# Kernel tuning notes

Measured on AMD Instinct MI355X. Metric: run time of the kernel, lower is better.

Reference implementation:

```python
import jax, jax.numpy as jnp
import numpy as np


def setup_inputs() -> dict:
    key = jax.random.key(0)
    ks = jax.random.split(key, 7)
    B, T, D, H, O = 64, 512, 256, 1024, 256
    s = 0.02  # small init scale for numerical stability of the recurrence
    return {
        "x": jax.random.normal(ks[0], (B, T, D), dtype=jnp.float32),
        "W_ih": jax.random.normal(ks[1], (4 * H, D), dtype=jnp.float32) * s,
        "W_hh": jax.random.normal(ks[2], (4 * H, H), dtype=jnp.float32) * s,
        "b_ih": jax.random.normal(ks[3], (4 * H,), dtype=jnp.float32) * s,
        "b_hh": jax.random.normal(ks[4], (4 * H,), dtype=jnp.float32) * s,
        "W_out": jax.random.normal(ks[5], (O, H), dtype=jnp.float32) * s,
        "b_out": jax.random.normal(ks[6], (O,), dtype=jnp.float32) * s,
    }


def reference(x, W_ih, W_hh, b_ih, b_hh, W_out, b_out):
    # x: [B, T, D]. Faithful to torch nn.LSTMCell gate order (i, f, g, o)
    # followed by a per-step Linear projection, future=0 path.
    B, T, D = x.shape
    H = W_hh.shape[1]

    # Precompute input contributions for all timesteps in one GEMM: [T, B, 4H]
    xg = jnp.einsum('btd,gd->tbg', x, W_ih) + b_ih + b_hh

    def step(carry, xg_t):
        h, c = carry
        gates = xg_t + h @ W_hh.T  # [B, 4H]
        i, f, g, o = jnp.split(gates, 4, axis=-1)
        i = jax.nn.sigmoid(i)
        f = jax.nn.sigmoid(f)
        g = jnp.tanh(g)
        o = jax.nn.sigmoid(o)
        c = f * c + i * g
        h = o * jnp.tanh(c)
        return (h, c), h

    h0 = jnp.zeros((B, H), dtype=x.dtype)
    c0 = jnp.zeros((B, H), dtype=x.dtype)
    _, hs = jax.lax.scan(step, (h0, c0), xg)  # hs: [T, B, H]

    # Per-step Linear, batched over time: [B, T, O]
    outputs = jnp.einsum('tbh,oh->bto', hs, W_out) + b_out
    return outputs
```

## Files before the change

kernel.cpp:

```cpp
#include <hip/hip_runtime.h>

#define B_ 64
#define T_ 512
#define D_ 256
#define H_ 1024
#define O_ 256
#define KTOT 1280
#define NBLK 256
#define NTHR 256

typedef __bf16 bf16x8 __attribute__((ext_vector_type(8)));
typedef float f32x4 __attribute__((ext_vector_type(4)));

__device__ __forceinline__ unsigned short f2bf(float f) {
    unsigned int u = __builtin_bit_cast(unsigned int, f);
    unsigned int r = (u + 0x7fffu + ((u >> 16) & 1u)) >> 16;
    return (unsigned short)r;
}
__device__ __forceinline__ float sigmoid_f(float x) { return 1.f / (1.f + __expf(-x)); }
__device__ __forceinline__ float tanh_f(float x)    { return 1.f - 2.f / (1.f + __expf(2.f * x)); }

#define ARR_OFF 0
#define RLS_OFF (T_ * NBLK)
#define SYNC_INTS (T_ * NBLK + T_ * 128)

__global__ void zero_sync(int* s) { s[blockIdx.x * 256 + threadIdx.x] = 0; }

__global__ __launch_bounds__(256) void pack_weights(
    const float* __restrict__ Wih, const float* __restrict__ Whh,
    const float* __restrict__ bih, const float* __restrict__ bhh,
    const float* __restrict__ Wout,
    unsigned short* __restrict__ Wp, float* __restrict__ bpk,
    unsigned short* __restrict__ Wo)
{
    int bid = blockIdx.x, tid = threadIdx.x;
    if (bid < 4096) {
        int g = bid & 3, j = (bid >> 2) & 3, hc = (bid >> 4) * 4 + j;
        int row = g * 1024 + hc;
        for (int e = tid; e < KTOT; e += 256) {
            float v = (e < D_) ? Wih[(size_t)row * D_ + e] : Whh[(size_t)row * H_ + (e - D_)];
            Wp[(size_t)bid * KTOT + e] = f2bf(v);
        }
        if (tid == 0) bpk[bid] = bih[row] + bhh[row];
    } else {
        int r = bid - 4096;
        for (int e = tid; e < H_; e += 256)
            Wo[(size_t)r * H_ + e] = f2bf(Wout[(size_t)r * H_ + e]);
    }
}

__global__ __launch_bounds__(256) void x_pack(const float* __restrict__ x,
                                              unsigned short* __restrict__ xt)
{
    int bid = blockIdx.x;
    int b = bid >> 9, t = bid & 511;
    int d = threadIdx.x;
    xt[((size_t)t * B_ + b) * D_ + d] = f2bf(x[(size_t)bid * D_ + d]);
}

__global__ __launch_bounds__(NTHR, 1) void lstm_scan(
    const unsigned short* __restrict__ Wp, const float* __restrict__ bpk,
    const unsigned short* __restrict__ xt, unsigned short* __restrict__ hs,
    int* __restrict__ sync)
{
    const int tid  = threadIdx.x;
    const int w    = tid >> 6, lane = tid & 63;
    const int blk  = blockIdx.x;
    const int n    = lane & 15, kg = lane >> 4;
    const int gq   = n & 3;
    const int hcol = blk * 4 + (n >> 2);
    const int m0   = w * 16;

    bf16x8 wf[40];
    {
        const bf16x8* wp8 = (const bf16x8*)(Wp + (size_t)(blk * 16 + n) * KTOT + kg * 8);
        #pragma unroll
        for (int kk = 0; kk < 40; ++kk) wf[kk] = wp8[kk * 4];
    }
    #pragma unroll
    for (int kk = 0; kk < 40; ++kk) asm volatile("" : "+v"(wf[kk]));

    const float bias = bpk[blk * 16 + n];

    float cc[4] = {0.f, 0.f, 0.f, 0.f};

    for (int t = 0; t < T_; ++t) {
        f32x4 ac[4];
        f32x4 z = {0.f, 0.f, 0.f, 0.f};
        ac[0] = z; ac[1] = z; ac[2] = z; ac[3] = z;

        {
            const bf16x8* ax = (const bf16x8*)(xt + ((size_t)t * B_ + m0 + n) * D_ + kg * 8);
            #pragma unroll
            for (int kk = 0; kk < 8; ++kk) {
                bf16x8 a = ax[kk * 4];
                ac[kk & 3] = __builtin_amdgcn_mfma_f32_16x16x32_bf16(a, wf[kk], ac[kk & 3], 0, 0, 0);
            }
        }

        if (t > 0) {
            const bool selfrel = (w == 0) && (blk == ((t - 1) & (NBLK - 1)));
            if (!selfrel) {
                const int* rw = sync + RLS_OFF + (size_t)(t - 1) * 128 + (((blk << 2) + w) & 7) * 16;
                while (__hip_atomic_load(rw, __ATOMIC_RELAXED, __HIP_MEMORY_SCOPE_AGENT) == 0) {}
            }

            const bf16x8* ah = (const bf16x8*)(hs + ((size_t)(t - 1) * B_ + m0 + n) * H_ + kg * 8);
            #pragma unroll
            for (int kk = 8; kk < 40; ++kk) {
                bf16x8 a = ah[(kk - 8) * 4];
                ac[kk & 3] = __builtin_amdgcn_mfma_f32_16x16x32_bf16(a, wf[kk], ac[kk & 3], 0, 0, 0);
            }
        }

        f32x4 g4 = (ac[0] + ac[1]) + (ac[2] + ac[3]);

        float hv[4];
        #pragma unroll
        for (int r = 0; r < 4; ++r) {
            float v  = g4[r] + bias;
            float v1 = __shfl_xor(v, 1);
            float v2 = __shfl_xor(v, 2);
            float v3 = __shfl_xor(v, 3);
            float iv = (gq == 0) ? v  : (gq == 1) ? v1 : (gq == 2) ? v2 : v3;
            float fv = (gq == 0) ? v1 : (gq == 1) ? v  : (gq == 2) ? v3 : v2;
            float gv = (gq == 0) ? v2 : (gq == 1) ? v3 : (gq == 2) ? v  : v1;
            float ov = (gq == 0) ? v3 : (gq == 1) ? v2 : (gq == 2) ? v1 : v;
            float is = sigmoid_f(iv), fs = sigmoid_f(fv), gt = tanh_f(gv), os = sigmoid_f(ov);
            float cn = fs * cc[r] + is * gt;
            cc[r] = cn;
            hv[r] = os * tanh_f(cn);
        }

        if (gq == 0) {
            #pragma unroll
            for (int r = 0; r < 4; ++r) {
                int br = m0 + kg * 4 + r;
                __hip_atomic_store(hs + ((size_t)t * B_ + br) * H_ + hcol, f2bf(hv[r]),
                                   __ATOMIC_RELAXED, __HIP_MEMORY_SCOPE_AGENT);
            }
        }
        asm volatile("s_waitcnt vmcnt(0)" ::: "memory");
        __syncthreads();

        if (tid == 0)
            __hip_atomic_store(sync + ARR_OFF + (size_t)t * NBLK + blk, 1,
                               __ATOMIC_RELAXED, __HIP_MEMORY_SCOPE_AGENT);

        if ((w == 0) && (blk == (t & (NBLK - 1))) && (t < T_ - 1)) {
            const int* ap = sync + ARR_OFF + (size_t)t * NBLK + lane * 4;
            for (;;) {
                int ok = 1;
                #pragma unroll
                for (int j = 0; j < 4; ++j) {
                    int idx = lane * 4 + j;
                    ok &= (idx == blk) |
                          (__hip_atomic_load(ap + j, __ATOMIC_RELAXED, __HIP_MEMORY_SCOPE_AGENT) != 0);
                }
                if (__all(ok)) break;
            }
            if (lane < 8)
                __hip_atomic_store(sync + RLS_OFF + (size_t)t * 128 + lane * 16, 1,
                                   __ATOMIC_RELAXED, __HIP_MEMORY_SCOPE_AGENT);
        }
    }
}

__global__ __launch_bounds__(256) void out_proj(
    const unsigned short* __restrict__ hs, const unsigned short* __restrict__ Wo,
    const float* __restrict__ bout, float* __restrict__ out)
{
    const int tid = threadIdx.x, wid = tid >> 6, lane = tid & 63;
    const int n = lane & 15, kg = lane >> 4;
    const int mb = blockIdx.x >> 2, nb = blockIdx.x & 3;
    const int m0 = mb * 64 + wid * 16;
    const int n0 = nb * 64;
    f32x4 acc[4];
    f32x4 z = {0.f, 0.f, 0.f, 0.f};
    acc[0] = z; acc[1] = z; acc[2] = z; acc[3] = z;
    const bf16x8* ap = (const bf16x8*)(hs + ((size_t)(m0 + n)) * H_ + kg * 8);
    #pragma unroll 2
    for (int kk = 0; kk < 32; ++kk) {
        bf16x8 a = ap[kk * 4];
        #pragma unroll
        for (int nt = 0; nt < 4; ++nt) {
            const bf16x8* bp8 = (const bf16x8*)(Wo + ((size_t)(n0 + nt * 16 + n)) * H_ + kg * 8);
            bf16x8 b = bp8[kk * 4];
            acc[nt] = __builtin_amdgcn_mfma_f32_16x16x32_bf16(a, b, acc[nt], 0, 0, 0);
        }
    }
    #pragma unroll
    for (int nt = 0; nt < 4; ++nt) {
        int col = n0 + nt * 16 + n;
        float bias = bout[col];
        #pragma unroll
        for (int r = 0; r < 4; ++r) {
            int m = m0 + kg * 4 + r;
            int tt = m >> 6, bb = m & 63;
            out[((size_t)bb * T_ + tt) * O_ + col] = acc[nt][r] + bias;
        }
    }
}

extern "C" void kernel_launch(void* const* d_in, const int* in_sizes, int n_in,
                              void* d_out, int out_size, void* d_ws, size_t ws_size,
                              hipStream_t stream)
{
    const float* x    = (const float*)d_in[0];
    const float* Wih  = (const float*)d_in[1];
    const float* Whh  = (const float*)d_in[2];
    const float* bih  = (const float*)d_in[3];
    const float* bhh  = (const float*)d_in[4];
    const float* Wout = (const float*)d_in[5];
    const float* bout = (const float*)d_in[6];
    float* out = (float*)d_out;

    char* ws = (char*)d_ws;
    unsigned short* Wp  = (unsigned short*)ws;  ws += (size_t)4096 * KTOT * 2;
    float*          bpk = (float*)ws;           ws += (size_t)4096 * 4;
    unsigned short* Wo  = (unsigned short*)ws;  ws += (size_t)O_ * H_ * 2;
    unsigned short* xt  = (unsigned short*)ws;  ws += (size_t)T_ * B_ * D_ * 2;
    unsigned short* hs  = (unsigned short*)ws;  ws += (size_t)T_ * B_ * H_ * 2;
    int*            syn = (int*)ws;             ws += (size_t)SYNC_INTS * 4;

    if (ws_size < (size_t)(ws - (char*)d_ws)) return;

    zero_sync<<<SYNC_INTS / 256, 256, 0, stream>>>(syn);
    pack_weights<<<4096 + 256, 256, 0, stream>>>(Wih, Whh, bih, bhh, Wout, Wp, bpk, Wo);
    x_pack<<<B_ * T_, 256, 0, stream>>>(x, xt);

    {
        const unsigned short* Wpc = Wp;
        const float*          bpc = bpk;
        const unsigned short* xtc = xt;
        unsigned short*       hsv = hs;
        int*                  syv = syn;
        void* args[5] = {(void*)&Wpc, (void*)&bpc, (void*)&xtc, (void*)&hsv, (void*)&syv};
        hipLaunchCooperativeKernel((void*)lstm_scan, dim3(NBLK), dim3(NTHR), args, 0, stream);
    }

    out_proj<<<(T_ * B_ / 64) * 4, 256, 0, stream>>>(hs, Wo, bout, out);
}
```

Baseline: 4.285 ms.

## Replace master-release barrier with per-wave byte flags polled by all waves

Drops the two-stage barrier, where one rotating block gathered per-block arrival flags and then published release flags. Each wave now writes its own byte flag after storing its h slice, and every wave polls all 1024 flags of the previous step directly, packed as ints, removing the __syncthreads and one global round trip per step. It also computes each gate's activation once per lane before shuffling instead of all four on every lane, and stages h through shared memory so one 8-byte store per row replaces four 2-byte stores; the weight packing order changes to match the new column layout. The cost is that every wave now polls 4KB of flags each step, adding memory traffic and contention.

```diff
diff --git a/kernel.cpp b/kernel.cpp
--- a/kernel.cpp
+++ b/kernel.cpp
@@ -20,9 +20,7 @@
 __device__ __forceinline__ float sigmoid_f(float x) { return 1.f / (1.f + __expf(-x)); }
 __device__ __forceinline__ float tanh_f(float x)    { return 1.f - 2.f / (1.f + __expf(2.f * x)); }
 
-#define ARR_OFF 0
-#define RLS_OFF (T_ * NBLK)
-#define SYNC_INTS (T_ * NBLK + T_ * 128)
+#define SYNC_INTS (T_ * 1024 / 4)
 
 __global__ void zero_sync(int* s) { s[blockIdx.x * 256 + threadIdx.x] = 0; }
 
@@ -35,7 +33,7 @@
 {
     int bid = blockIdx.x, tid = threadIdx.x;
     if (bid < 4096) {
-        int g = bid & 3, j = (bid >> 2) & 3, hc = (bid >> 4) * 4 + j;
+        int g = bid & 3, hc = bid >> 2;
         int row = g * 1024 + hc;
         for (int e = tid; e < KTOT; e += 256) {
             float v = (e < D_) ? Wih[(size_t)row * D_ + e] : Whh[(size_t)row * H_ + (e - D_)];
@@ -68,8 +66,11 @@
     const int blk  = blockIdx.x;
     const int n    = lane & 15, kg = lane >> 4;
     const int gq   = n & 3;
-    const int hcol = blk * 4 + (n >> 2);
     const int m0   = w * 16;
+
+    unsigned char* arrB = (unsigned char*)sync;
+
+    __shared__ unsigned short st[4][16][4];
 
     bf16x8 wf[40];
     {
@@ -99,10 +100,15 @@
         }
 
         if (t > 0) {
-            const bool selfrel = (w == 0) && (blk == ((t - 1) & (NBLK - 1)));
-            if (!selfrel) {
-                const int* rw = sync + RLS_OFF + (size_t)(t - 1) * 128 + (((blk << 2) + w) & 7) * 16;
-                while (__hip_atomic_load(rw, __ATOMIC_RELAXED, __HIP_MEMORY_SCOPE_AGENT) == 0) {}
+            const int* ap = (const int*)(arrB + (size_t)(t - 1) * 1024) + lane * 4;
+            for (;;) {
+                int v0 = __hip_atomic_load(ap + 0, __ATOMIC_RELAXED, __HIP_MEMORY_SCOPE_AGENT);
+                int v1 = __hip_atomic_load(ap + 1, __ATOMIC_RELAXED, __HIP_MEMORY_SCOPE_AGENT);
+                int v2 = __hip_atomic_load(ap + 2, __ATOMIC_RELAXED, __HIP_MEMORY_SCOPE_AGENT);
+                int v3 = __hip_atomic_load(ap + 3, __ATOMIC_RELAXED, __HIP_MEMORY_SCOPE_AGENT);
+                int ok = (v0 == 0x01010101) & (v1 == 0x01010101) &
+                         (v2 == 0x01010101) & (v3 == 0x01010101);
+                if (__all(ok)) break;
             }
 
             const bf16x8* ah = (const bf16x8*)(hs + ((size_t)(t - 1) * B_ + m0 + n) * H_ + kg * 8);
@@ -115,54 +121,33 @@
 
         f32x4 g4 = (ac[0] + ac[1]) + (ac[2] + ac[3]);
 
-        float hv[4];
         #pragma unroll
         for (int r = 0; r < 4; ++r) {
-            float v  = g4[r] + bias;
-            float v1 = __shfl_xor(v, 1);
-            float v2 = __shfl_xor(v, 2);
-            float v3 = __shfl_xor(v, 3);
-            float iv = (gq == 0) ? v  : (gq == 1) ? v1 : (gq == 2) ? v2 : v3;
-            float fv = (gq == 0) ? v1 : (gq == 1) ? v  : (gq == 2) ? v3 : v2;
-            float gv = (gq == 0) ? v2 : (gq == 1) ? v3 : (gq == 2) ? v  : v1;
-            float ov = (gq == 0) ? v3 : (gq == 1) ? v2 : (gq == 2) ? v1 : v;
-            float is = sigmoid_f(iv), fs = sigmoid_f(fv), gt = tanh_f(gv), os = sigmoid_f(ov);
-            float cn = fs * cc[r] + is * gt;
+            float v   = g4[r] + bias;
+            float act = (gq == 2) ? tanh_f(v) : sigmoid_f(v);
+            float a1 = __shfl_xor(act, 1);
+            float a2 = __shfl_xor(act, 2);
+            float a3 = __shfl_xor(act, 3);
+            float ia = (gq == 0) ? act : (gq == 1) ? a1 : (gq == 2) ? a2 : a3;
+            float fa = (gq == 0) ? a1 : (gq == 1) ? act : (gq == 2) ? a3 : a2;
+            float ga = (gq == 0) ? a2 : (gq == 1) ? a3 : (gq == 2) ? act : a1;
+            float oa = (gq == 0) ? a3 : (gq == 1) ? a2 : (gq == 2) ? a1 : act;
+            float cn = fa * cc[r] + ia * ga;
             cc[r] = cn;
-            hv[r] = os * tanh_f(cn);
-        }
-
-        if (gq == 0) {
-            #pragma unroll
-            for (int r = 0; r < 4; ++r) {
-                int br = m0 + kg * 4 + r;
-                __hip_atomic_store(hs + ((size_t)t * B_ + br) * H_ + hcol, f2bf(hv[r]),
-                                   __ATOMIC_RELAXED, __HIP_MEMORY_SCOPE_AGENT);
-            }
+            float hv = oa * tanh_f(cn);
+            if (gq == 0) st[w][kg * 4 + r][n >> 2] = f2bf(hv);
+        }
+
+        asm volatile("s_waitcnt lgkmcnt(0)" ::: "memory");
+        if (lane < 16) {
+            unsigned long long pv = *(const unsigned long long*)&st[w][lane][0];
+            __hip_atomic_store((unsigned long long*)(hs + ((size_t)t * B_ + m0 + lane) * H_ + blk * 4),
+                               pv, __ATOMIC_RELAXED, __HIP_MEMORY_SCOPE_AGENT);
         }
         asm volatile("s_waitcnt vmcnt(0)" ::: "memory");
-        __syncthreads();
-
-        if (tid == 0)
-            __hip_atomic_store(sync + ARR_OFF + (size_t)t * NBLK + blk, 1,
+        if (lane == 0 && t < T_ - 1)
+            __hip_atomic_store(arrB + (size_t)t * 1024 + blk * 4 + w, (unsigned char)1,
                                __ATOMIC_RELAXED, __HIP_MEMORY_SCOPE_AGENT);
-
-        if ((w == 0) && (blk == (t & (NBLK - 1))) && (t < T_ - 1)) {
-            const int* ap = sync + ARR_OFF + (size_t)t * NBLK + lane * 4;
-            for (;;) {
-                int ok = 1;
-                #pragma unroll
-                for (int j = 0; j < 4; ++j) {
-                    int idx = lane * 4 + j;
-                    ok &= (idx == blk) |
-                          (__hip_atomic_load(ap + j, __ATOMIC_RELAXED, __HIP_MEMORY_SCOPE_AGENT) != 0);
-                }
-                if (__all(ok)) break;
-            }
-            if (lane < 8)
-                __hip_atomic_store(sync + RLS_OFF + (size_t)t * 128 + lane * 16, 1,
-                                   __ATOMIC_RELAXED, __HIP_MEMORY_SCOPE_AGENT);
-        }
     }
 }
 
```

Result: slower. 5.147 ms (+20.1%).
